# Kernel tuning notes

Hardware: AMD Instinct MI355X
Metric: run time of the kernel (lower is better)

Reference implementation:

```python
import jax, jax.numpy as jnp
import numpy as np

INPUT_DIM = 64
LATENT_DIM = 512
K = 32
BATCH = 262144


def xavier_uniform(key, shape):
    fan_out, fan_in = shape
    limit = float(np.sqrt(6.0 / (fan_in + fan_out)))
    return jax.random.uniform(key, shape, jnp.float32, -limit, limit)


def setup_inputs() -> dict:
    key = jax.random.key(0)
    kx, ke, kd = jax.random.split(key, 3)
    x = jax.random.normal(kx, (BATCH, INPUT_DIM), dtype=jnp.float32)
    enc_W = xavier_uniform(ke, (LATENT_DIM, INPUT_DIM))  # torch Linear weight layout [out, in]
    enc_b = jnp.zeros((LATENT_DIM,), jnp.float32)
    dec_W = xavier_uniform(kd, (INPUT_DIM, LATENT_DIM))
    dec_b = jnp.zeros((INPUT_DIM,), jnp.float32)
    return {"x": x, "enc_W": enc_W, "enc_b": enc_b, "dec_W": dec_W, "dec_b": dec_b}


def reference(x, enc_W, enc_b, dec_W, dec_b):
    # encode: linear -> relu -> top-k mask
    z = jax.nn.relu(x @ enc_W.T + enc_b)                 # [B, LATENT_DIM]
    vals, idx = jax.lax.top_k(z, K)                      # [B, K]
    rows = jnp.arange(z.shape[0])[:, None]               # [B, 1]
    z_sparse = jnp.zeros_like(z).at[rows, idx].set(vals) # scatter top-k back
    # decode
    x_hat = z_sparse @ dec_W.T + dec_b                   # [B, INPUT_DIM]
    return x_hat, z_sparse
```

## Files before the change

### kernel.cpp

```cpp
#include <hip/hip_runtime.h>


#define BATCH 262144
#define IND   64
#define LAT   512
#define TOPK  32
#define RPB   128
#define TR    32
#define NTT   (RPB / TR)
#define CCAP  128
#define EPSC  4.2e-3f
#define NB    32
#define NBPAD 36

typedef __attribute__((ext_vector_type(8))) short short8;
typedef __attribute__((ext_vector_type(4))) float f32x4;

__device__ __forceinline__ unsigned short f2bf(float f) {
  unsigned u = __float_as_uint(f);
  unsigned r = ((u >> 16) & 1u) + 0x7FFFu;
  return (unsigned short)((u + r) >> 16);
}
__device__ __forceinline__ float bfbits2f(unsigned short s) {
  return __uint_as_float(((unsigned)s) << 16);
}
__device__ __forceinline__ float edgef(int t) {
  return __uint_as_float((unsigned)(1888 + t) << 19);
}
__device__ __forceinline__ short8 pack8(float4 a, float4 b) {
  short8 r;
  r[0] = (short)f2bf(a.x); r[1] = (short)f2bf(a.y);
  r[2] = (short)f2bf(a.z); r[3] = (short)f2bf(a.w);
  r[4] = (short)f2bf(b.x); r[5] = (short)f2bf(b.y);
  r[6] = (short)f2bf(b.z); r[7] = (short)f2bf(b.w);
  return r;
}
__device__ __forceinline__ void split8(const float* p, short8& h, short8& l) {
  #pragma unroll
  for (int i = 0; i < 8; i++) {
    float v = p[i];
    unsigned short hb = f2bf(v);
    float r = v - bfbits2f(hb);
    h[i] = (short)hb;
    l[i] = (short)f2bf(r);
  }
}
__device__ __forceinline__ float exact_dot64(const float* __restrict__ wr,
                                             const float* xr) {
  float s = 0.0f;
  #pragma unroll 1
  for (int g = 0; g < 2; g++) {
    const float4 w0 = *(const float4*)(wr + 32*g);
    const float4 w1 = *(const float4*)(wr + 32*g + 4);
    const float4 w2 = *(const float4*)(wr + 32*g + 8);
    const float4 w3 = *(const float4*)(wr + 32*g + 12);
    const float4 w4 = *(const float4*)(wr + 32*g + 16);
    const float4 w5 = *(const float4*)(wr + 32*g + 20);
    const float4 w6 = *(const float4*)(wr + 32*g + 24);
    const float4 w7 = *(const float4*)(wr + 32*g + 28);
    const float* xk = xr + 32*g;
    s = fmaf(xk[0],  w0.x, s); s = fmaf(xk[1],  w0.y, s);
    s = fmaf(xk[2],  w0.z, s); s = fmaf(xk[3],  w0.w, s);
    s = fmaf(xk[4],  w1.x, s); s = fmaf(xk[5],  w1.y, s);
    s = fmaf(xk[6],  w1.z, s); s = fmaf(xk[7],  w1.w, s);
    s = fmaf(xk[8],  w2.x, s); s = fmaf(xk[9],  w2.y, s);
    s = fmaf(xk[10], w2.z, s); s = fmaf(xk[11], w2.w, s);
    s = fmaf(xk[12], w3.x, s); s = fmaf(xk[13], w3.y, s);
    s = fmaf(xk[14], w3.z, s); s = fmaf(xk[15], w3.w, s);
    s = fmaf(xk[16], w4.x, s); s = fmaf(xk[17], w4.y, s);
    s = fmaf(xk[18], w4.z, s); s = fmaf(xk[19], w4.w, s);
    s = fmaf(xk[20], w5.x, s); s = fmaf(xk[21], w5.y, s);
    s = fmaf(xk[22], w5.z, s); s = fmaf(xk[23], w5.w, s);
    s = fmaf(xk[24], w6.x, s); s = fmaf(xk[25], w6.y, s);
    s = fmaf(xk[26], w6.z, s); s = fmaf(xk[27], w6.w, s);
    s = fmaf(xk[28], w7.x, s); s = fmaf(xk[29], w7.y, s);
    s = fmaf(xk[30], w7.z, s); s = fmaf(xk[31], w7.w, s);
  }
  return s;
}

__global__ __launch_bounds__(256, 2)
void sae_fused(const float* __restrict__ xg,
               const float* __restrict__ encW,
               const float* __restrict__ encB,
               const float* __restrict__ decW,
               const float* __restrict__ decB,
               float* __restrict__ out_xhat,
               float* __restrict__ out_z)
{
  __shared__ unsigned       hist[TR][NBPAD];
  __shared__ unsigned short zsp[TR][520];
  __shared__ float    xtile[TR][68];
  __shared__ unsigned short cidx[TR][CCAP];
  __shared__ float    rowlo[TR];
  __shared__ float    xabs[TR];
  __shared__ float    xlo0[TR];
  __shared__ float    xinvw[TR];
  __shared__ float    xwid[TR];
  __shared__ int      ccnt[TR];
  __shared__ int      degen[TR];
  __shared__ int      wmax_i;
  __shared__ int      fbmask;

  const int tid  = threadIdx.x;
  const int w    = tid >> 6;
  const int lane = tid & 63;
  const int c    = lane & 15;
  const int q    = lane >> 4;

  if (tid == 0) wmax_i = 0;
  __syncthreads();

  short8 beh[8][2];
  float  lmax = 0.0f;
  #pragma unroll
  for (int n = 0; n < 8; n++)
    #pragma unroll
    for (int ks = 0; ks < 2; ks++) {
      const float* p = encW + (size_t)(128*w + 16*n + c)*IND + 32*ks + 8*q;
      float4 a = *(const float4*)p, b = *(const float4*)(p + 4);
      lmax = fmaxf(lmax, fmaxf(fmaxf(fabsf(a.x), fabsf(a.y)), fmaxf(fabsf(a.z), fabsf(a.w))));
      lmax = fmaxf(lmax, fmaxf(fmaxf(fabsf(b.x), fabsf(b.y)), fmaxf(fabsf(b.z), fabsf(b.w))));
      beh[n][ks] = pack8(a, b);
    }
  atomicMax(&wmax_i, __float_as_int(lmax));

  short8 bd[16];
  #pragma unroll 1
  for (int g = 0; g < 4; g++)
    #pragma unroll
    for (int j = 0; j < 4; j++) {
      const int ks = 4*g + j;
      const float* p = decW + (size_t)(16*w + c)*LAT + 32*ks + 8*q;
      bd[ks] = pack8(*(const float4*)p, *(const float4*)(p + 4));
    }

  float ebias[8];
  #pragma unroll
  for (int n = 0; n < 8; n++) ebias[n] = encB[128*w + 16*n + c];
  const float dbias = decB[16*w + c];
  __syncthreads();
  const float wmaxf = __int_as_float(wmax_i);

  #pragma unroll 1
  for (int t = 0; t < NTT; t++) {
    const int rowbase = blockIdx.x * RPB + t * TR;

    {
      uint4 z4 = {0,0,0,0};
      uint4* hp = (uint4*)&hist[0][0];
      hp[tid] = z4;
      if (tid < 32) hp[256 + tid] = z4;
      uint4* zp = (uint4*)&zsp[0][0];
      #pragma unroll
      for (int i = 0; i < 8; i++) zp[tid + 256*i] = z4;
      if (tid < 32) zp[2048 + tid] = z4;
      if (tid < TR) { ccnt[tid] = 0; degen[tid] = 0; }
      if (tid == 0) fbmask = 0;
    }
    {
      const int row = tid >> 3, sub = tid & 7;
      const f32x4* gp = (const f32x4*)(xg + (size_t)(rowbase + row)*IND) + 2*sub;
      f32x4 a = __builtin_nontemporal_load(gp);
      f32x4 b = __builtin_nontemporal_load(gp + 1);
      *(f32x4*)&xtile[row][8*sub]     = a;
      *(f32x4*)&xtile[row][8*sub + 4] = b;
      float s  = fabsf(a.x)+fabsf(a.y)+fabsf(a.z)+fabsf(a.w)
               + fabsf(b.x)+fabsf(b.y)+fabsf(b.z)+fabsf(b.w);
      float s2 = a.x*a.x+a.y*a.y+a.z*a.z+a.w*a.w
               + b.x*b.x+b.y*b.y+b.z*b.z+b.w*b.w;
      s  += __shfl_xor(s, 1);  s  += __shfl_xor(s, 2);  s  += __shfl_xor(s, 4);
      s2 += __shfl_xor(s2, 1); s2 += __shfl_xor(s2, 2); s2 += __shfl_xor(s2, 4);
      if (sub == 0) {
        xabs[row] = s;
        const float sig = 0.058926f * sqrtf(s2);
        xlo0[row]  = fmaxf(0.7f * sig, edgef(1));
        xwid[row]  = (2.5f / (float)NB) * sig;
        xinvw[row] = (float)NB / fmaxf(2.5f * sig, 1e-20f);
      }
    }
    __syncthreads();

    f32x4 acc[2][8];
    #pragma unroll
    for (int m2 = 0; m2 < 2; m2++)
      #pragma unroll
      for (int n = 0; n < 8; n++) acc[m2][n] = (f32x4){0.f,0.f,0.f,0.f};

    #pragma unroll
    for (int m2 = 0; m2 < 2; m2++) {
      const float* xr = &xtile[16*m2 + c][0];
      short8 a0h, a0l, a1h, a1l;
      split8(xr + 8*q,      a0h, a0l);
      split8(xr + 32 + 8*q, a1h, a1l);
      #pragma unroll
      for (int n = 0; n < 8; n++) {
        acc[m2][n] = __builtin_amdgcn_mfma_f32_16x16x32_bf16(a0h, beh[n][0], acc[m2][n], 0,0,0);
        acc[m2][n] = __builtin_amdgcn_mfma_f32_16x16x32_bf16(a0l, beh[n][0], acc[m2][n], 0,0,0);
        acc[m2][n] = __builtin_amdgcn_mfma_f32_16x16x32_bf16(a1h, beh[n][1], acc[m2][n], 0,0,0);
        acc[m2][n] = __builtin_amdgcn_mfma_f32_16x16x32_bf16(a1l, beh[n][1], acc[m2][n], 0,0,0);
      }
    }
    {
      float flo[2][4], fiw[2][4];
      #pragma unroll
      for (int m2 = 0; m2 < 2; m2++)
        #pragma unroll
        for (int r = 0; r < 4; r++) {
          flo[m2][r] = xlo0[16*m2 + 4*q + r];
          fiw[m2][r] = xinvw[16*m2 + 4*q + r];
        }
      #pragma unroll
      for (int m2 = 0; m2 < 2; m2++)
        #pragma unroll
        for (int n = 0; n < 8; n++)
          #pragma unroll
          for (int r = 0; r < 4; r++) {
            float v = fmaxf(acc[m2][n][r] + ebias[n], 0.0f);
            acc[m2][n][r] = v;
            if (v >= flo[m2][r]) {
              const int row = 16*m2 + 4*q + r;
              int k = (int)((v - flo[m2][r]) * fiw[m2][r]);
              k = min(k, NB-1);
              atomicAdd(&hist[row][k], 1u);
            }
          }
    }
    __syncthreads();

    #pragma unroll 1
    for (int rr = 0; rr < 8; rr++) {
      const int row = 8*w + rr;
      uint4 h = {0,0,0,0};
      if (lane < 8) h = *(const uint4*)&hist[row][4*lane];
      int T = (int)(h.x + h.y + h.z + h.w);
      int I = T;
      #pragma unroll
      for (int d = 1; d < 8; d <<= 1) {
        int t2 = __shfl_down(I, d);
        if (lane + d < 8) I += t2;
      }
      const int I0 = __shfl(I, 0);
      if (I0 < TOPK) {
        if (lane == 0) atomicOr(&fbmask, (int)(1u << row));
      } else {
        unsigned long long msk = __ballot(I >= TOPK);
        const int ls = __popcll(msk) - 1;
        const int Il = __shfl(I, ls);
        const int hx = __shfl((int)h.x, ls);
        const int hy = __shfl((int)h.y, ls);
        const int hz = __shfl((int)h.z, ls);
        const int s1 = Il - hx, s2 = s1 - hy, s3 = s2 - hz;
        const int t8 = (s3 >= TOPK) ? 4*ls+3 : (s2 >= TOPK) ? 4*ls+2
                     : (s1 >= TOPK) ? 4*ls+1 : 4*ls;
        if (lane == 0) {
          const float eps2 = EPSC * wmaxf * xabs[row] + 1e-7f;
          rowlo[row] = fmaxf(xlo0[row] + (float)t8 * xwid[row] - 2.0f*eps2, 1e-30f);
        }
      }
    }
    __syncthreads();

    if (fbmask) {
      unsigned* fb = &hist[0][0];
      unsigned fbm = (unsigned)fbmask;
      while (fbm) {
        const int R = (int)__ffs(fbm) - 1;
        fbm &= fbm - 1;
        fb[tid] = 0;
        __syncthreads();
        if ((lane >> 4) == ((R >> 2) & 3)) {
          const int m2R = R >> 4, rR = R & 3;
          #pragma unroll
          for (int m2 = 0; m2 < 2; m2++)
            #pragma unroll
            for (int r = 0; r < 4; r++)
              if (m2 == m2R && r == rR) {
                #pragma unroll
                for (int n = 0; n < 8; n++) {
                  float v = acc[m2][n][r];
                  int k8 = (int)(__float_as_uint(v) >> 19) - 1888;
                  k8 = max(0, min(255, k8));
                  atomicAdd(&fb[k8], 1u);
                }
              }
        }
        __syncthreads();
        if (w == 0) {
          uint4 h = *(const uint4*)&fb[4*lane];
          int T = (int)(h.x + h.y + h.z + h.w);
          int I = T;
          #pragma unroll
          for (int d = 1; d < 64; d <<= 1) {
            int t2 = __shfl_down(I, d);
            if (lane + d < 64) I += t2;
          }
          const int I0  = __shfl(I, 0);
          const int hx0 = __shfl((int)h.x, 0);
          if (I0 - hx0 < TOPK) {
            if (lane == 0) { degen[R] = 1; rowlo[R] = edgef(1); }
          } else {
            unsigned long long msk = __ballot(I >= TOPK);
            const int ls = __popcll(msk) - 1;
            const int Il = __shfl(I, ls);
            const int hx = __shfl((int)h.x, ls);
            const int hy = __shfl((int)h.y, ls);
            const int hz = __shfl((int)h.z, ls);
            const int s1 = Il - hx, s2 = s1 - hy, s3 = s2 - hz;
            const int t8 = (s3 >= TOPK) ? 4*ls+3 : (s2 >= TOPK) ? 4*ls+2
                         : (s1 >= TOPK) ? 4*ls+1 : 4*ls;
            if (lane == 0) {
              const float eps2 = EPSC * wmaxf * xabs[R] + 1e-7f;
              rowlo[R] = fmaxf(edgef(t8) - 2.0f*eps2, 1e-30f);
            }
          }
        }
        __syncthreads();
      }
    }

    #pragma unroll
    for (int m2 = 0; m2 < 2; m2++)
      #pragma unroll
      for (int r = 0; r < 4; r++) {
        const int row = 16*m2 + 4*q + r;
        const float lo = rowlo[row];
        const int dg = degen[row];
        #pragma unroll
        for (int n = 0; n < 8; n++) {
          const float v = acc[m2][n][r];
          if (v >= lo) {
            if (dg) {
              zsp[row][128*w + 16*n + c] = f2bf(v);
            } else {
              int slot = atomicAdd(&ccnt[row], 1);
              if (slot < CCAP) cidx[row][slot] = (unsigned short)(128*w + 16*n + c);
            }
          }
        }
      }
    __syncthreads();

    #pragma unroll 1
    for (int rr = 0; rr < 8; rr++) {
      const int row = 8*w + rr;
      if (degen[row]) continue;
      const int m  = min(ccnt[row], CCAP);
      const int mA = min(m, 64);
      const int mB = m - mA;
      const float* xr = &xtile[row][0];

      int ciA = 0xFFFF; float sA = -1e30f;
      {
        const int js = (lane < mA) ? (int)cidx[row][lane] : 0;
        float s = exact_dot64(encW + (size_t)js * IND, xr);
        s += encB[js];
        s = fmaxf(s, 0.0f);
        if (lane < mA) { sA = s; ciA = js; }
      }
      int ciB = 0xFFFF; float sB = -1e30f;
      if (mB > 0) {
        const int js = (lane < mB) ? (int)cidx[row][64 + lane] : 0;
        float s = exact_dot64(encW + (size_t)js * IND, xr);
        s += encB[js];
        s = fmaxf(s, 0.0f);
        if (lane < mB) { sB = s; ciB = js; }
      }

      int rank0 = 0, rank1 = 0;
      for (int jj = 0; jj < mA; jj++) {
        const float vj = __shfl(sA, jj);
        const int   ij = __shfl(ciA, jj);
        rank0 += (vj > sA || (vj == sA && ij < ciA)) ? 1 : 0;
        rank1 += (vj > sB || (vj == sB && ij < ciB)) ? 1 : 0;
      }
      for (int jj = 0; jj < mB; jj++) {
        const float vj = __shfl(sB, jj);
        const int   ij = __shfl(ciB, jj);
        rank0 += (vj > sA || (vj == sA && ij < ciA)) ? 1 : 0;
        rank1 += (vj > sB || (vj == sB && ij < ciB)) ? 1 : 0;
      }
      if (lane < mA && rank0 < TOPK) zsp[row][ciA] = f2bf(sA);
      if (mB > 0 && lane < mB && rank1 < TOPK) zsp[row][ciB] = f2bf(sB);
    }
    __syncthreads();

    #pragma unroll 1
    for (int rr = 0; rr < 8; rr++) {
      const int row = 8*w + rr;
      const unsigned short* zr = &zsp[row][8*lane];
      f32x4 o0, o1;
      o0.x = bfbits2f(zr[0]); o0.y = bfbits2f(zr[1]); o0.z = bfbits2f(zr[2]); o0.w = bfbits2f(zr[3]);
      o1.x = bfbits2f(zr[4]); o1.y = bfbits2f(zr[5]); o1.z = bfbits2f(zr[6]); o1.w = bfbits2f(zr[7]);
      f32x4* orow = (f32x4*)(out_z + (size_t)(rowbase + row)*LAT + 8*lane);
      __builtin_nontemporal_store(o0, orow);
      __builtin_nontemporal_store(o1, orow + 1);
    }
    {
      f32x4 acc2[2];
      acc2[0] = (f32x4){0.f,0.f,0.f,0.f};
      acc2[1] = (f32x4){0.f,0.f,0.f,0.f};
      #pragma unroll
      for (int ks = 0; ks < 16; ks++) {
        short8 a0 = *(const short8*)&zsp[c][32*ks + 8*q];
        short8 a1 = *(const short8*)&zsp[16 + c][32*ks + 8*q];
        acc2[0] = __builtin_amdgcn_mfma_f32_16x16x32_bf16(a0, bd[ks], acc2[0], 0,0,0);
        acc2[1] = __builtin_amdgcn_mfma_f32_16x16x32_bf16(a1, bd[ks], acc2[1], 0,0,0);
      }
      #pragma unroll
      for (int m2 = 0; m2 < 2; m2++)
        #pragma unroll
        for (int r = 0; r < 4; r++)
          out_xhat[(size_t)(rowbase + 16*m2 + 4*q + r)*IND + 16*w + c] = acc2[m2][r] + dbias;
    }
    __syncthreads();
  }
}

extern "C" void kernel_launch(void* const* d_in, const int* in_sizes, int n_in,
                              void* d_out, int out_size, void* d_ws, size_t ws_size,
                              hipStream_t stream) {
  (void)in_sizes; (void)n_in; (void)out_size; (void)d_ws; (void)ws_size;
  const float* x    = (const float*)d_in[0];
  const float* encW = (const float*)d_in[1];
  const float* encB = (const float*)d_in[2];
  const float* decW = (const float*)d_in[3];
  const float* decB = (const float*)d_in[4];
  float* out_xhat = (float*)d_out;
  float* out_z    = out_xhat + (size_t)BATCH * IND;

  dim3 grid(BATCH / RPB), block(256);
  sae_fused<<<grid, block, 0, stream>>>(x, encW, encB, decW, decB, out_xhat, out_z);
}
```

Measured before the change: 1.649 ms.

## Raise occupancy by reloading decoder weights per tile and aliasing shared buffers

Raises the launch bound from 2 to 3 blocks per SIMD-group and frees the 64 VGPRs that held the packed decoder weights. Those weights are now reloaded from global/L2 and packed to bf16 inside the decode step of every tile. The histogram, fallback and candidate-index shared arrays are placed in a union to cut LDS per block, and the second candidate batch is split into its own branch so the common case skips it. The aim is more resident waves to hide latency, at the cost of repeated decW loads and pack work per tile plus possible register spills under the tighter bound.

```diff
diff --git a/kernel.cpp b/kernel.cpp
--- a/kernel.cpp
+++ b/kernel.cpp
@@ -79,7 +79,7 @@
   return s;
 }
 
-__global__ __launch_bounds__(256, 2)
+__global__ __launch_bounds__(256, 3)
 void sae_fused(const float* __restrict__ xg,
                const float* __restrict__ encW,
                const float* __restrict__ encB,
@@ -88,10 +88,13 @@
                float* __restrict__ out_xhat,
                float* __restrict__ out_z)
 {
-  __shared__ unsigned       hist[TR][NBPAD];
+  __shared__ union {
+    unsigned       hist[TR][NBPAD];
+    unsigned       fb[256];
+    unsigned short cidx[TR][CCAP];
+  } hc;
   __shared__ unsigned short zsp[TR][520];
   __shared__ float    xtile[TR][68];
-  __shared__ unsigned short cidx[TR][CCAP];
   __shared__ float    rowlo[TR];
   __shared__ float    xabs[TR];
   __shared__ float    xlo0[TR];
@@ -125,16 +128,6 @@
     }
   atomicMax(&wmax_i, __float_as_int(lmax));
 
-  short8 bd[16];
-  #pragma unroll 1
-  for (int g = 0; g < 4; g++)
-    #pragma unroll
-    for (int j = 0; j < 4; j++) {
-      const int ks = 4*g + j;
-      const float* p = decW + (size_t)(16*w + c)*LAT + 32*ks + 8*q;
-      bd[ks] = pack8(*(const float4*)p, *(const float4*)(p + 4));
-    }
-
   float ebias[8];
   #pragma unroll
   for (int n = 0; n < 8; n++) ebias[n] = encB[128*w + 16*n + c];
@@ -148,7 +141,7 @@
 
     {
       uint4 z4 = {0,0,0,0};
-      uint4* hp = (uint4*)&hist[0][0];
+      uint4* hp = (uint4*)&hc.hist[0][0];
       hp[tid] = z4;
       if (tid < 32) hp[256 + tid] = z4;
       uint4* zp = (uint4*)&zsp[0][0];
@@ -222,7 +215,7 @@
               const int row = 16*m2 + 4*q + r;
               int k = (int)((v - flo[m2][r]) * fiw[m2][r]);
               k = min(k, NB-1);
-              atomicAdd(&hist[row][k], 1u);
+              atomicAdd(&hc.hist[row][k], 1u);
             }
           }
     }
@@ -232,7 +225,7 @@
     for (int rr = 0; rr < 8; rr++) {
       const int row = 8*w + rr;
       uint4 h = {0,0,0,0};
-      if (lane < 8) h = *(const uint4*)&hist[row][4*lane];
+      if (lane < 8) h = *(const uint4*)&hc.hist[row][4*lane];
       int T = (int)(h.x + h.y + h.z + h.w);
       int I = T;
       #pragma unroll
@@ -262,7 +255,7 @@
     __syncthreads();
 
     if (fbmask) {
-      unsigned* fb = &hist[0][0];
+      unsigned* fb = &hc.fb[0];
       unsigned fbm = (unsigned)fbmask;
       while (fbm) {
         const int R = (int)__ffs(fbm) - 1;
@@ -334,7 +327,7 @@
               zsp[row][128*w + 16*n + c] = f2bf(v);
             } else {
               int slot = atomicAdd(&ccnt[row], 1);
-              if (slot < CCAP) cidx[row][slot] = (unsigned short)(128*w + 16*n + c);
+              if (slot < CCAP) hc.cidx[row][slot] = (unsigned short)(128*w + 16*n + c);
             }
           }
         }
@@ -352,36 +345,46 @@
 
       int ciA = 0xFFFF; float sA = -1e30f;
       {
-        const int js = (lane < mA) ? (int)cidx[row][lane] : 0;
+        const int js = (lane < mA) ? (int)hc.cidx[row][lane] : 0;
         float s = exact_dot64(encW + (size_t)js * IND, xr);
         s += encB[js];
         s = fmaxf(s, 0.0f);
         if (lane < mA) { sA = s; ciA = js; }
       }
-      int ciB = 0xFFFF; float sB = -1e30f;
-      if (mB > 0) {
-        const int js = (lane < mB) ? (int)cidx[row][64 + lane] : 0;
-        float s = exact_dot64(encW + (size_t)js * IND, xr);
-        s += encB[js];
-        s = fmaxf(s, 0.0f);
-        if (lane < mB) { sB = s; ciB = js; }
-      }
-
-      int rank0 = 0, rank1 = 0;
-      for (int jj = 0; jj < mA; jj++) {
-        const float vj = __shfl(sA, jj);
-        const int   ij = __shfl(ciA, jj);
-        rank0 += (vj > sA || (vj == sA && ij < ciA)) ? 1 : 0;
-        rank1 += (vj > sB || (vj == sB && ij < ciB)) ? 1 : 0;
-      }
-      for (int jj = 0; jj < mB; jj++) {
-        const float vj = __shfl(sB, jj);
-        const int   ij = __shfl(ciB, jj);
-        rank0 += (vj > sA || (vj == sA && ij < ciA)) ? 1 : 0;
-        rank1 += (vj > sB || (vj == sB && ij < ciB)) ? 1 : 0;
-      }
-      if (lane < mA && rank0 < TOPK) zsp[row][ciA] = f2bf(sA);
-      if (mB > 0 && lane < mB && rank1 < TOPK) zsp[row][ciB] = f2bf(sB);
+
+      if (mB == 0) {
+        int rank0 = 0;
+        for (int jj = 0; jj < mA; jj++) {
+          const float vj = __shfl(sA, jj);
+          const int   ij = __shfl(ciA, jj);
+          rank0 += (vj > sA || (vj == sA && ij < ciA)) ? 1 : 0;
+        }
+        if (lane < mA && rank0 < TOPK) zsp[row][ciA] = f2bf(sA);
+      } else {
+        int ciB = 0xFFFF; float sB = -1e30f;
+        {
+          const int js = (lane < mB) ? (int)hc.cidx[row][64 + lane] : 0;
+          float s = exact_dot64(encW + (size_t)js * IND, xr);
+          s += encB[js];
+          s = fmaxf(s, 0.0f);
+          if (lane < mB) { sB = s; ciB = js; }
+        }
+        int rank0 = 0, rank1 = 0;
+        for (int jj = 0; jj < mA; jj++) {
+          const float vj = __shfl(sA, jj);
+          const int   ij = __shfl(ciA, jj);
+          rank0 += (vj > sA || (vj == sA && ij < ciA)) ? 1 : 0;
+          rank1 += (vj > sB || (vj == sB && ij < ciB)) ? 1 : 0;
+        }
+        for (int jj = 0; jj < mB; jj++) {
+          const float vj = __shfl(sB, jj);
+          const int   ij = __shfl(ciB, jj);
+          rank0 += (vj > sA || (vj == sA && ij < ciA)) ? 1 : 0;
+          rank1 += (vj > sB || (vj == sB && ij < ciB)) ? 1 : 0;
+        }
+        if (lane < mA && rank0 < TOPK) zsp[row][ciA] = f2bf(sA);
+        if (lane < mB && rank1 < TOPK) zsp[row][ciB] = f2bf(sB);
+      }
     }
     __syncthreads();
 
@@ -400,12 +403,23 @@
       f32x4 acc2[2];
       acc2[0] = (f32x4){0.f,0.f,0.f,0.f};
       acc2[1] = (f32x4){0.f,0.f,0.f,0.f};
-      #pragma unroll
-      for (int ks = 0; ks < 16; ks++) {
-        short8 a0 = *(const short8*)&zsp[c][32*ks + 8*q];
-        short8 a1 = *(const short8*)&zsp[16 + c][32*ks + 8*q];
-        acc2[0] = __builtin_amdgcn_mfma_f32_16x16x32_bf16(a0, bd[ks], acc2[0], 0,0,0);
-        acc2[1] = __builtin_amdgcn_mfma_f32_16x16x32_bf16(a1, bd[ks], acc2[1], 0,0,0);
+      const float* pw = decW + (size_t)(16*w + c)*LAT + 8*q;
+      #pragma unroll 1
+      for (int g = 0; g < 4; g++) {
+        short8 bd4[4];
+        #pragma unroll
+        for (int j = 0; j < 4; j++) {
+          const float* p = pw + 32*(4*g + j);
+          bd4[j] = pack8(*(const float4*)p, *(const float4*)(p + 4));
+        }
+        #pragma unroll
+        for (int j = 0; j < 4; j++) {
+          const int ks = 4*g + j;
+          short8 a0 = *(const short8*)&zsp[c][32*ks + 8*q];
+          short8 a1 = *(const short8*)&zsp[16 + c][32*ks + 8*q];
+          acc2[0] = __builtin_amdgcn_mfma_f32_16x16x32_bf16(a0, bd4[j], acc2[0], 0,0,0);
+          acc2[1] = __builtin_amdgcn_mfma_f32_16x16x32_bf16(a1, bd4[j], acc2[1], 0,0,0);
+        }
       }
       #pragma unroll
       for (int m2 = 0; m2 < 2; m2++)
```

Result: slower. 1.874 ms (+13.6%).
